# Kernel optimization log

Measured on AMD Instinct MI355X. Metric: run time of the kernel, lower is better.

Reference implementation:

```python
import jax, jax.numpy as jnp
import numpy as np
import math

B, T, C, H = 4, 4096, 1024, 16
D = C // H

def setup_inputs() -> dict:
    key = jax.random.key(0)
    k1, k2, k3, k4, k5 = jax.random.split(key, 5)
    s = 1.0 / math.sqrt(C)
    return {
        "x": jax.random.normal(k1, (B, T, C), dtype=jnp.float32),
        "W_qkv": jax.random.normal(k2, (C, 3 * C), dtype=jnp.float32) * s,
        "b_qkv": jax.random.normal(k3, (3 * C,), dtype=jnp.float32) * 0.01,
        "W_out": jax.random.normal(k4, (C, C), dtype=jnp.float32) * s,
        "b_out": jax.random.normal(k5, (C,), dtype=jnp.float32) * 0.01,
    }

def reference(x, W_qkv, b_qkv, W_out, b_out):
    qkv = x @ W_qkv + b_qkv                      # (B,T,3C)
    q, k, v = jnp.split(qkv, 3, axis=2)
    q = q.reshape(B, T, H, D)
    k = k.reshape(B, T, H, D)
    v = v.reshape(B, T, H, D)
    # attention over the HEAD axis per (B,T): scores (B,T,H,H)
    att = jnp.einsum('bthd,btgd->bthg', q, k) / math.sqrt(D)
    att = jax.nn.softmax(att, axis=-1)
    out = jnp.einsum('bthg,btgd->bthd', att, v)  # (B,T,H,D)
    out = out.reshape(B, T, C)
    return out @ W_out + b_out
```

## Files before the change

### kernel.cpp

```cpp
#include <hip/hip_runtime.h>
#include <cstdint>
#include <cstddef>

constexpr int Bc = 4;
constexpr int Tc = 4096;
constexpr int Cc = 1024;
constexpr int Hc = 16;
constexpr int Dc = 64;
constexpr int Mc = Bc * Tc;
constexpr int N1c = 3 * Cc;
constexpr int Kc = Cc;
constexpr int KBc = Kc / 32;

typedef __bf16 bf16x8 __attribute__((ext_vector_type(8)));
typedef float  f32x4  __attribute__((ext_vector_type(4)));
typedef __attribute__((address_space(1))) uint32_t gu32;
typedef __attribute__((address_space(3))) uint32_t lu32;

__device__ __forceinline__ float bf2f(unsigned short u) {
    return __uint_as_float(((unsigned)u) << 16);
}
__device__ __forceinline__ unsigned short f2bf(float f) {
    unsigned u = __float_as_uint(f);
    u += 0x7FFF + ((u >> 16) & 1);
    return (unsigned short)(u >> 16);
}

__device__ __forceinline__ void load_lds16(const void* g, void* l) {
    __builtin_amdgcn_global_load_lds((gu32*)(uintptr_t)g, (lu32*)(uintptr_t)l, 16, 0, 0);
}


__global__ void convert_x_packed(const float* __restrict__ x,
                                 unsigned short* __restrict__ Ap) {
    const int w = threadIdx.x >> 6, lane = threadIdx.x & 63;
    const int t = blockIdx.x * 4 + w;
    const int mb = t >> 5, kb = t & 31;
    const int r = lane >> 2, c = lane & 3;
    const float* src = x + (size_t)(mb * 16 + r) * Kc + kb * 32 + c * 8;
    float4 f0 = *(const float4*)src;
    float4 f1 = *(const float4*)(src + 4);
    unsigned short u[8];
    u[0] = f2bf(f0.x); u[1] = f2bf(f0.y); u[2] = f2bf(f0.z); u[3] = f2bf(f0.w);
    u[4] = f2bf(f1.x); u[5] = f2bf(f1.y); u[6] = f2bf(f1.z); u[7] = f2bf(f1.w);
    *(uint4*)(Ap + (size_t)t * 512 + (c * 16 + r) * 8) = *(uint4*)u;
}

__global__ void transpose_convert_packed(const float* __restrict__ W,
                                         unsigned short* __restrict__ Bp,
                                         int K, int N) {
    __shared__ float tile[32][33];
    const int tx = threadIdx.x, ty = threadIdx.y;
    const int n0 = blockIdx.x * 32, k0 = blockIdx.y * 32;
    for (int i = ty; i < 32; i += 8)
        tile[i][tx] = W[(size_t)(k0 + i) * N + n0 + tx];
    __syncthreads();
    const int t = ty * 32 + tx;
    const int h = t >> 7, rr = t & 127, lane = rr >> 1, half = rr & 1;
    const int fq = lane >> 4, fn = lane & 15;
    unsigned short u[4];
    #pragma unroll
    for (int j = 0; j < 4; ++j)
        u[j] = f2bf(tile[fq * 8 + half * 4 + j][h * 16 + fn]);
    size_t tileIdx = (size_t)((n0 >> 4) + h) * (K >> 5) + (k0 >> 5);
    *(uint2*)(Bp + tileIdx * 512 + lane * 8 + half * 4) = *(uint2*)u;
}

template <bool OUT_BF16>
__global__ __launch_bounds__(256, 4) void lds_gemm_kernel(
    const unsigned short* __restrict__ Ap,
    const unsigned short* __restrict__ Bp,
    const float* __restrict__ bias,
    void* __restrict__ Cout,
    int M, int N, int K, int NB) {
    __shared__ unsigned short sA[8 * 512];
    __shared__ unsigned short sB[8 * 512];
    const int KB = K >> 5;
    const int MB = M >> 7;
    const int id   = blockIdx.x;
    const int xcd  = id & 7;
    const int per  = id >> 3;
    const int MSTR = MB >> 3;
    const int byl  = per & 7;
    const int bx   = (per >> 3) % NB;
    const int pass = per / (8 * NB);
    const int by   = xcd * MSTR + pass * 8 + byl;

    const int w    = threadIdx.x >> 6;
    const int lane = threadIdx.x & 63;
    const int m0 = by * 128;
    const int n0 = bx * 128;
    const int wm = (w >> 1) * 64;
    const int wn = (w & 1) * 64;

    const unsigned short* gA0 = Ap + ((size_t)(by * 8 + w    ) * KB) * 512 + lane * 8;
    const unsigned short* gA1 = Ap + ((size_t)(by * 8 + w + 4) * KB) * 512 + lane * 8;
    const unsigned short* gB0 = Bp + ((size_t)(bx * 8 + w    ) * KB) * 512 + lane * 8;
    const unsigned short* gB1 = Bp + ((size_t)(bx * 8 + w + 4) * KB) * 512 + lane * 8;
    unsigned short* lA0 = sA + (w    ) * 512;
    unsigned short* lA1 = sA + (w + 4) * 512;
    unsigned short* lB0 = sB + (w    ) * 512;
    unsigned short* lB1 = sB + (w + 4) * 512;

    const unsigned short* aP = sA + (wm >> 4) * 512 + lane * 8;
    const unsigned short* bP = sB + (wn >> 4) * 512 + lane * 8;

    const f32x4 zero4 = {0.f, 0.f, 0.f, 0.f};
    f32x4 acc[4][4];
    #pragma unroll
    for (int i = 0; i < 4; ++i)
        #pragma unroll
        for (int j = 0; j < 4; ++j) acc[i][j] = zero4;

    #pragma unroll 1
    for (int kb = 0; kb < KB; ++kb) {
        load_lds16(gA0, lA0);
        load_lds16(gA1, lA1);
        load_lds16(gB0, lB0);
        load_lds16(gB1, lB1);
        gA0 += 512; gA1 += 512; gB0 += 512; gB1 += 512;
        __syncthreads();

        bf16x8 af[4], bfr[4];
        #pragma unroll
        for (int mi = 0; mi < 4; ++mi) af[mi]  = *(const bf16x8*)(aP + mi * 512);
        #pragma unroll
        for (int ni = 0; ni < 4; ++ni) bfr[ni] = *(const bf16x8*)(bP + ni * 512);
        #pragma unroll
        for (int mi = 0; mi < 4; ++mi)
            #pragma unroll
            for (int ni = 0; ni < 4; ++ni)
                acc[mi][ni] = __builtin_amdgcn_mfma_f32_16x16x32_bf16(
                    af[mi], bfr[ni], acc[mi][ni], 0, 0, 0);
        __syncthreads();
    }

    const int fr = lane & 15;
    const int fq = lane >> 4;
    #pragma unroll
    for (int mi = 0; mi < 4; ++mi) {
        #pragma unroll
        for (int ni = 0; ni < 4; ++ni) {
            int row = m0 + wm + mi * 16 + fq * 4;
            int col = n0 + wn + ni * 16 + fr;
            float bb = bias[col];
            #pragma unroll
            for (int r = 0; r < 4; ++r) {
                float v = acc[mi][ni][r] + bb;
                if (OUT_BF16)
                    ((unsigned short*)Cout)[(size_t)(row + r) * N + col] = f2bf(v);
                else
                    ((float*)Cout)[(size_t)(row + r) * N + col] = v;
            }
        }
    }
}

__global__ __launch_bounds__(256) void attn_mfma_kernel(
    const unsigned short* __restrict__ qkv,
    unsigned short* __restrict__ attP) {
    __shared__ char smem[4 * 3584];
    const int w    = threadIdx.x >> 6;
    const int lane = threadIdx.x & 63;
    const int m    = lane & 15;
    const int q    = lane >> 4;
    const int row  = blockIdx.x * 4 + w;
    unsigned short* sV = (unsigned short*)(smem + w * 3584);
    float*          sP = (float*)(smem + w * 3584 + 2304);

    const unsigned short* src = qkv + (size_t)row * 3072;

    bf16x8 aq0 = *(const bf16x8*)(src + m * 64 + q * 8);
    bf16x8 aq1 = *(const bf16x8*)(src + m * 64 + 32 + q * 8);
    bf16x8 bk0 = *(const bf16x8*)(src + 1024 + m * 64 + q * 8);
    bf16x8 bk1 = *(const bf16x8*)(src + 1024 + m * 64 + 32 + q * 8);

    #pragma unroll
    for (int t = 0; t < 2; ++t) {
        int G = t * 64 + lane;
        int r = G >> 3, p = G & 7;
        *(uint4*)(sV + r * 72 + p * 8) = *(const uint4*)(src + 2048 + G * 8);
    }

    f32x4 s = {0.f, 0.f, 0.f, 0.f};
    s = __builtin_amdgcn_mfma_f32_16x16x32_bf16(aq0, bk0, s, 0, 0, 0);
    s = __builtin_amdgcn_mfma_f32_16x16x32_bf16(aq1, bk1, s, 0, 0, 0);

    #pragma unroll
    for (int r = 0; r < 4; ++r) {
        float t0 = s[r] * 0.125f;
        float mx = t0;
        mx = fmaxf(mx, __shfl_xor(mx, 1));
        mx = fmaxf(mx, __shfl_xor(mx, 2));
        mx = fmaxf(mx, __shfl_xor(mx, 4));
        mx = fmaxf(mx, __shfl_xor(mx, 8));
        float e = __expf(t0 - mx);
        float su = e;
        su += __shfl_xor(su, 1);
        su += __shfl_xor(su, 2);
        su += __shfl_xor(su, 4);
        su += __shfl_xor(su, 8);
        sP[(q * 4 + r) * 20 + m] = e / su;
    }
    __syncthreads();

    const float* pr = sP + m * 20 + (q & 1) * 8;
    float4 pf0 = *(const float4*)(pr);
    float4 pf1 = *(const float4*)(pr + 4);
    const bool act = (q < 2);
    union { unsigned short u[8]; bf16x8 b; } pa;
    pa.u[0] = act ? f2bf(pf0.x) : 0;
    pa.u[1] = act ? f2bf(pf0.y) : 0;
    pa.u[2] = act ? f2bf(pf0.z) : 0;
    pa.u[3] = act ? f2bf(pf0.w) : 0;
    pa.u[4] = act ? f2bf(pf1.x) : 0;
    pa.u[5] = act ? f2bf(pf1.y) : 0;
    pa.u[6] = act ? f2bf(pf1.z) : 0;
    pa.u[7] = act ? f2bf(pf1.w) : 0;

    const unsigned short* vb = sV + (q & 1) * 8 * 72;
    const size_t tileBase = (size_t)(row >> 4) * 32 * 512;
    const int fr_tok = row & 15;
    #pragma unroll
    for (int c4 = 0; c4 < 4; ++c4) {
        union { unsigned short u[8]; bf16x8 b; } vf;
        #pragma unroll
        for (int j = 0; j < 8; ++j) vf.u[j] = vb[j * 72 + c4 * 16 + m];
        f32x4 o = {0.f, 0.f, 0.f, 0.f};
        o = __builtin_amdgcn_mfma_f32_16x16x32_bf16(pa.b, vf.b, o, 0, 0, 0);
        #pragma unroll
        for (int r = 0; r < 4; ++r) {
            int col = (q * 4 + r) * 64 + c4 * 16 + m;
            size_t off = tileBase + (size_t)(col >> 5) * 512
                       + (((col >> 3) & 3) * 16 + fr_tok) * 8 + (col & 7);
            attP[off] = f2bf(o[r]);
        }
    }
}

extern "C" void kernel_launch(void* const* d_in, const int* in_sizes, int n_in,
                              void* d_out, int out_size, void* d_ws, size_t ws_size,
                              hipStream_t stream) {
    const float* x    = (const float*)d_in[0];
    const float* Wqkv = (const float*)d_in[1];
    const float* bqkv = (const float*)d_in[2];
    const float* Wout = (const float*)d_in[3];
    const float* bout = (const float*)d_in[4];
    float* out = (float*)d_out;

    char* ws = (char*)d_ws;
    unsigned short* xp   = (unsigned short*)ws;                 ws += (size_t)Mc * Kc * 2;
    unsigned short* Wqkp = (unsigned short*)ws;                 ws += (size_t)N1c * Kc * 2;
    unsigned short* Wop  = (unsigned short*)ws;                 ws += (size_t)Cc * Kc * 2;
    unsigned short* qkv  = (unsigned short*)ws;
    unsigned short* attP = xp;

    convert_x_packed<<<(Mc / 16) * KBc / 4, 256, 0, stream>>>(x, xp);
    transpose_convert_packed<<<dim3(N1c / 32, Kc / 32), dim3(32, 8), 0, stream>>>(Wqkv, Wqkp, Kc, N1c);
    transpose_convert_packed<<<dim3(Cc / 32, Kc / 32), dim3(32, 8), 0, stream>>>(Wout, Wop, Kc, Cc);
    lds_gemm_kernel<true><<<(N1c / 128) * (Mc / 128), 256, 0, stream>>>(
        xp, Wqkp, bqkv, qkv, Mc, N1c, Kc, N1c / 128);
    attn_mfma_kernel<<<Mc / 4, 256, 0, stream>>>(qkv, attP);
    lds_gemm_kernel<false><<<(Cc / 128) * (Mc / 128), 256, 0, stream>>>(
        attP, Wop, bout, out, Mc, Cc, Kc, Cc / 128);
}
```

Measured before the change: 295.9 us.

## Double GEMM K-step per barrier and emit transposed V from QKV GEMM epilogue

```diff
diff --git a/kernel.cpp b/kernel.cpp
--- a/kernel.cpp
+++ b/kernel.cpp
@@ -66,17 +66,19 @@
     *(uint2*)(Bp + tileIdx * 512 + lane * 8 + half * 4) = *(uint2*)u;
 }
 
-template <bool OUT_BF16>
+template <bool OUT_BF16, bool VSPLIT>
 __global__ __launch_bounds__(256, 4) void lds_gemm_kernel(
     const unsigned short* __restrict__ Ap,
     const unsigned short* __restrict__ Bp,
     const float* __restrict__ bias,
     void* __restrict__ Cout,
+    unsigned short* __restrict__ vT,
     int M, int N, int K, int NB) {
-    __shared__ unsigned short sA[8 * 512];
-    __shared__ unsigned short sB[8 * 512];
-    const int KB = K >> 5;
-    const int MB = M >> 7;
+    __shared__ unsigned short sA[16 * 512];
+    __shared__ unsigned short sB[16 * 512];
+    const int KB  = K >> 5;
+    const int KB2 = K >> 6;
+    const int MB  = M >> 7;
     const int id   = blockIdx.x;
     const int xcd  = id & 7;
     const int per  = id >> 3;
@@ -97,13 +99,13 @@
     const unsigned short* gA1 = Ap + ((size_t)(by * 8 + w + 4) * KB) * 512 + lane * 8;
     const unsigned short* gB0 = Bp + ((size_t)(bx * 8 + w    ) * KB) * 512 + lane * 8;
     const unsigned short* gB1 = Bp + ((size_t)(bx * 8 + w + 4) * KB) * 512 + lane * 8;
-    unsigned short* lA0 = sA + (w    ) * 512;
-    unsigned short* lA1 = sA + (w + 4) * 512;
-    unsigned short* lB0 = sB + (w    ) * 512;
-    unsigned short* lB1 = sB + (w + 4) * 512;
-
-    const unsigned short* aP = sA + (wm >> 4) * 512 + lane * 8;
-    const unsigned short* bP = sB + (wn >> 4) * 512 + lane * 8;
+    unsigned short* lA0 = sA + (w * 2) * 512;
+    unsigned short* lA1 = sA + ((w + 4) * 2) * 512;
+    unsigned short* lB0 = sB + (w * 2) * 512;
+    unsigned short* lB1 = sB + ((w + 4) * 2) * 512;
+
+    const unsigned short* aP = sA + ((wm >> 4) * 2) * 512 + lane * 8;
+    const unsigned short* bP = sB + ((wn >> 4) * 2) * 512 + lane * 8;
 
     const f32x4 zero4 = {0.f, 0.f, 0.f, 0.f};
     f32x4 acc[4][4];
@@ -113,25 +115,34 @@
         for (int j = 0; j < 4; ++j) acc[i][j] = zero4;
 
     #pragma unroll 1
-    for (int kb = 0; kb < KB; ++kb) {
-        load_lds16(gA0, lA0);
-        load_lds16(gA1, lA1);
-        load_lds16(gB0, lB0);
-        load_lds16(gB1, lB1);
-        gA0 += 512; gA1 += 512; gB0 += 512; gB1 += 512;
+    for (int kb = 0; kb < KB2; ++kb) {
+        load_lds16(gA0,       lA0);
+        load_lds16(gA0 + 512, lA0 + 512);
+        load_lds16(gA1,       lA1);
+        load_lds16(gA1 + 512, lA1 + 512);
+        load_lds16(gB0,       lB0);
+        load_lds16(gB0 + 512, lB0 + 512);
+        load_lds16(gB1,       lB1);
+        load_lds16(gB1 + 512, lB1 + 512);
+        gA0 += 1024; gA1 += 1024; gB0 += 1024; gB1 += 1024;
         __syncthreads();
 
-        bf16x8 af[4], bfr[4];
-        #pragma unroll
-        for (int mi = 0; mi < 4; ++mi) af[mi]  = *(const bf16x8*)(aP + mi * 512);
-        #pragma unroll
-        for (int ni = 0; ni < 4; ++ni) bfr[ni] = *(const bf16x8*)(bP + ni * 512);
-        #pragma unroll
-        for (int mi = 0; mi < 4; ++mi)
+        #pragma unroll
+        for (int ks = 0; ks < 2; ++ks) {
+            bf16x8 af[4], bfr[4];
+            #pragma unroll
+            for (int mi = 0; mi < 4; ++mi)
+                af[mi]  = *(const bf16x8*)(aP + (mi * 2 + ks) * 512);
             #pragma unroll
             for (int ni = 0; ni < 4; ++ni)
-                acc[mi][ni] = __builtin_amdgcn_mfma_f32_16x16x32_bf16(
-                    af[mi], bfr[ni], acc[mi][ni], 0, 0, 0);
+                bfr[ni] = *(const bf16x8*)(bP + (ni * 2 + ks) * 512);
+            #pragma unroll
+            for (int mi = 0; mi < 4; ++mi)
+                #pragma unroll
+                for (int ni = 0; ni < 4; ++ni)
+                    acc[mi][ni] = __builtin_amdgcn_mfma_f32_16x16x32_bf16(
+                        af[mi], bfr[ni], acc[mi][ni], 0, 0, 0);
+        }
         __syncthreads();
     }
 
@@ -144,13 +155,20 @@
             int row = m0 + wm + mi * 16 + fq * 4;
             int col = n0 + wn + ni * 16 + fr;
             float bb = bias[col];
-            #pragma unroll
-            for (int r = 0; r < 4; ++r) {
-                float v = acc[mi][ni][r] + bb;
-                if (OUT_BF16)
-                    ((unsigned short*)Cout)[(size_t)(row + r) * N + col] = f2bf(v);
-                else
-                    ((float*)Cout)[(size_t)(row + r) * N + col] = v;
+            if (VSPLIT && col >= 2048) {
+                int g = (col - 2048) >> 6, d = (col - 2048) & 63;
+                #pragma unroll
+                for (int r = 0; r < 4; ++r)
+                    vT[(size_t)(row + r) * 1024 + d * 16 + g] = f2bf(acc[mi][ni][r] + bb);
+            } else {
+                #pragma unroll
+                for (int r = 0; r < 4; ++r) {
+                    float v = acc[mi][ni][r] + bb;
+                    if (OUT_BF16)
+                        ((unsigned short*)Cout)[(size_t)(row + r) * N + col] = f2bf(v);
+                    else
+                        ((float*)Cout)[(size_t)(row + r) * N + col] = v;
+                }
             }
         }
     }
@@ -158,15 +176,15 @@
 
 __global__ __launch_bounds__(256) void attn_mfma_kernel(
     const unsigned short* __restrict__ qkv,
+    const unsigned short* __restrict__ vT,
     unsigned short* __restrict__ attP) {
-    __shared__ char smem[4 * 3584];
+    __shared__ float sPm[4][16 * 20];
     const int w    = threadIdx.x >> 6;
     const int lane = threadIdx.x & 63;
     const int m    = lane & 15;
     const int q    = lane >> 4;
     const int row  = blockIdx.x * 4 + w;
-    unsigned short* sV = (unsigned short*)(smem + w * 3584);
-    float*          sP = (float*)(smem + w * 3584 + 2304);
+    float* sP = sPm[w];
 
     const unsigned short* src = qkv + (size_t)row * 3072;
 
@@ -175,12 +193,11 @@
     bf16x8 bk0 = *(const bf16x8*)(src + 1024 + m * 64 + q * 8);
     bf16x8 bk1 = *(const bf16x8*)(src + 1024 + m * 64 + 32 + q * 8);
 
-    #pragma unroll
-    for (int t = 0; t < 2; ++t) {
-        int G = t * 64 + lane;
-        int r = G >> 3, p = G & 7;
-        *(uint4*)(sV + r * 72 + p * 8) = *(const uint4*)(src + 2048 + G * 8);
-    }
+    const unsigned short* vsrc = vT + (size_t)row * 1024;
+    bf16x8 vt[4];
+    #pragma unroll
+    for (int c4 = 0; c4 < 4; ++c4)
+        vt[c4] = *(const bf16x8*)(vsrc + (c4 * 16 + m) * 16 + q * 8);
 
     f32x4 s = {0.f, 0.f, 0.f, 0.f};
     s = __builtin_amdgcn_mfma_f32_16x16x32_bf16(aq0, bk0, s, 0, 0, 0);
@@ -218,16 +235,12 @@
     pa.u[6] = act ? f2bf(pf1.z) : 0;
     pa.u[7] = act ? f2bf(pf1.w) : 0;
 
-    const unsigned short* vb = sV + (q & 1) * 8 * 72;
     const size_t tileBase = (size_t)(row >> 4) * 32 * 512;
     const int fr_tok = row & 15;
     #pragma unroll
     for (int c4 = 0; c4 < 4; ++c4) {
-        union { unsigned short u[8]; bf16x8 b; } vf;
-        #pragma unroll
-        for (int j = 0; j < 8; ++j) vf.u[j] = vb[j * 72 + c4 * 16 + m];
         f32x4 o = {0.f, 0.f, 0.f, 0.f};
-        o = __builtin_amdgcn_mfma_f32_16x16x32_bf16(pa.b, vf.b, o, 0, 0, 0);
+        o = __builtin_amdgcn_mfma_f32_16x16x32_bf16(pa.b, vt[c4], o, 0, 0, 0);
         #pragma unroll
         for (int r = 0; r < 4; ++r) {
             int col = (q * 4 + r) * 64 + c4 * 16 + m;
@@ -252,15 +265,16 @@
     unsigned short* xp   = (unsigned short*)ws;                 ws += (size_t)Mc * Kc * 2;
     unsigned short* Wqkp = (unsigned short*)ws;                 ws += (size_t)N1c * Kc * 2;
     unsigned short* Wop  = (unsigned short*)ws;                 ws += (size_t)Cc * Kc * 2;
-    unsigned short* qkv  = (unsigned short*)ws;
+    unsigned short* qkv  = (unsigned short*)ws;                 ws += (size_t)Mc * N1c * 2;
+    unsigned short* vT   = (unsigned short*)ws;
     unsigned short* attP = xp;
 
     convert_x_packed<<<(Mc / 16) * KBc / 4, 256, 0, stream>>>(x, xp);
     transpose_convert_packed<<<dim3(N1c / 32, Kc / 32), dim3(32, 8), 0, stream>>>(Wqkv, Wqkp, Kc, N1c);
     transpose_convert_packed<<<dim3(Cc / 32, Kc / 32), dim3(32, 8), 0, stream>>>(Wout, Wop, Kc, Cc);
-    lds_gemm_kernel<true><<<(N1c / 128) * (Mc / 128), 256, 0, stream>>>(
-        xp, Wqkp, bqkv, qkv, Mc, N1c, Kc, N1c / 128);
-    attn_mfma_kernel<<<Mc / 4, 256, 0, stream>>>(qkv, attP);
-    lds_gemm_kernel<false><<<(Cc / 128) * (Mc / 128), 256, 0, stream>>>(
-        attP, Wop, bout, out, Mc, Cc, Kc, Cc / 128);
-}
+    lds_gemm_kernel<true, true><<<(N1c / 128) * (Mc / 128), 256, 0, stream>>>(
+        xp, Wqkp, bqkv, qkv, vT, Mc, N1c, Kc, N1c / 128);
+    attn_mfma_kernel<<<Mc / 4, 256, 0, stream>>>(qkv, vT, attP);
+    lds_gemm_kernel<false, false><<<(Cc / 128) * (Mc / 128), 256, 0, stream>>>(
+        attP, Wop, bout, out, nullptr, Mc, Cc, Kc, Cc / 128);
+}
```

After: 331.6 us. 12.1% more time.
